# Performance work log

Measured on AMD Instinct MI355X. Metric: run time of the kernel, lower is better.

Reference implementation:

```python
import jax, jax.numpy as jnp
import numpy as np

D = 128  # h_dim == in_dim

def _gat_layer(h, d, src, dst, n_dst, W, U, V, a):
    # h: [N_src, Din], d: [E, 1], src/dst: [E]
    z = h @ W.T          # [N_src, D]
    zi = h @ U.T         # [N_src, D]
    t = d @ V.T          # [E, 1]
    Dh = W.shape[0]
    # attn_fc on concat([z_src, z_dst, t]) split into three partial dots
    e = z[src] @ a[:Dh] + z[dst] @ a[Dh:2 * Dh] + t[:, 0] * a[2 * Dh]
    e = jax.nn.leaky_relu(e)  # [E]
    # segment softmax over incoming edges of each dst node
    m = jax.ops.segment_max(e, dst, num_segments=n_dst)
    ex = jnp.exp(e - m[dst])
    s = jax.ops.segment_sum(ex, dst, num_segments=n_dst)
    alpha = ex / s[dst]  # [E]
    zn = jax.ops.segment_sum(alpha[:, None] * z[src], dst, num_segments=n_dst)
    return jax.nn.relu(zi[:n_dst] + zn)


def setup_inputs() -> dict:
    key = jax.random.key(0)
    ks = jax.random.split(key, 16)
    N0, ND0, ND1 = 100000, 40000, 20000
    E0, E1 = 640000, 320000
    sc = 1.0 / np.sqrt(D)
    inp = {
        "attr": jax.random.normal(ks[0], (N0, D), jnp.float32),
        "d0": jax.random.normal(ks[1], (E0, 1), jnp.float32),
        "d1": jax.random.normal(ks[2], (E1, 1), jnp.float32),
        "src0": jax.random.randint(ks[3], (E0,), 0, N0, jnp.int32),
        "dst0": jax.random.randint(ks[4], (E0,), 0, ND0, jnp.int32),
        "src1": jax.random.randint(ks[5], (E1,), 0, ND0, jnp.int32),
        "dst1": jax.random.randint(ks[6], (E1,), 0, ND1, jnp.int32),
        "n_dst0": ND0,
        "n_dst1": ND1,
        "W0": jax.random.normal(ks[7], (D, D), jnp.float32) * sc,
        "U0": jax.random.normal(ks[8], (D, D), jnp.float32) * sc,
        "V0": jax.random.normal(ks[9], (1, 1), jnp.float32),
        "a0": jax.random.normal(ks[10], (2 * D + 1,), jnp.float32) * sc,
        "W1": jax.random.normal(ks[11], (D, D), jnp.float32) * sc,
        "U1": jax.random.normal(ks[12], (D, D), jnp.float32) * sc,
        "V1": jax.random.normal(ks[13], (1, 1), jnp.float32),
        "a1": jax.random.normal(ks[14], (2 * D + 1,), jnp.float32) * sc,
    }
    return inp


def reference(attr, d0, d1, W0, U0, V0, a0, W1, U1, V1, a1,
              src0, dst0, src1, dst1, n_dst0, n_dst1):
    h = _gat_layer(attr, d0, src0, dst0, n_dst0, W0, U0, V0, a0)
    h = _gat_layer(h, d1, src1, dst1, n_dst1, W1, U1, V1, a1)
    return h
```

## Files before the change

kernel.cpp:

```cpp
#include <hip/hip_runtime.h>
#include <math.h>


#define D 128

typedef __bf16 bf16x8 __attribute__((ext_vector_type(8)));
typedef float f32x4 __attribute__((ext_vector_type(4)));

static __device__ __forceinline__ float lrelu(float x) {
  return x >= 0.f ? x : 0.01f * x;
}
static __device__ __forceinline__ unsigned short f2bf(float v) {
  unsigned int u = __float_as_uint(v);
  u += 0x7fffu + ((u >> 16) & 1u);
  return (unsigned short)(u >> 16);
}
static __device__ __forceinline__ float bf2f(unsigned short b) {
  return __uint_as_float((unsigned int)b << 16);
}

static __device__ __forceinline__ float4 loadV4(const float* p) {
  return *(const float4*)p;
}
static __device__ __forceinline__ float4 loadV4(const unsigned short* p) {
  ushort4 t = *(const ushort4*)p;
  return make_float4(bf2f(t.x), bf2f(t.y), bf2f(t.z), bf2f(t.w));
}
static __device__ __forceinline__ void storeV4(float* p, float4 v) {
  *(float4*)p = v;
}
static __device__ __forceinline__ void storeV4(unsigned short* p, float4 v) {
  ushort4 t;
  t.x = f2bf(v.x);
  t.y = f2bf(v.y);
  t.z = f2bf(v.z);
  t.w = f2bf(v.w);
  *(ushort4*)p = t;
}
static __device__ __forceinline__ void storeZi(float* p, float v) { *p = v; }
static __device__ __forceinline__ void storeZi(unsigned short* p, float v) {
  *p = f2bf(v);
}

static __device__ __forceinline__ int swz(int row, int colb) {
  return row * 256 + (colb ^ ((row & 7) << 4));
}

__global__ __launch_bounds__(256) void cvt4_kernel(
    const float* __restrict__ s0, const float* __restrict__ s1,
    const float* __restrict__ s2, const float* __restrict__ s3,
    __bf16* __restrict__ dst) {
  int idx = blockIdx.x * 256 + threadIdx.x;
  const float* s = (idx < 16384) ? s0
                   : (idx < 32768) ? s1
                   : (idx < 49152) ? s2 : s3;
  dst[idx] = (__bf16)s[idx & 16383];
}

__global__ void zero_int_kernel(int* __restrict__ p, int n) {
  int i = blockIdx.x * 256 + threadIdx.x;
  if (i < n) p[i] = 0;
}

static __device__ __forceinline__ void stageA(const float* A, int rblk,
                                              int rlim, int t,
                                              unsigned char* ldsA) {
  const char* base = (const char*)A + (size_t)rblk * 512;
#pragma unroll
  for (int g = 0; g < 8; ++g) {
    int sb = g * 4096 + t * 16;
    float4 v = make_float4(0.f, 0.f, 0.f, 0.f);
    if (rblk + (sb >> 9) < rlim) v = *(const float4*)(base + sb);
    int db = sb >> 1;
    int row = db >> 8, colb = db & 255;
    ushort4 o;
    o.x = f2bf(v.x);
    o.y = f2bf(v.y);
    o.z = f2bf(v.z);
    o.w = f2bf(v.w);
    *(ushort4*)(&ldsA[swz(row, colb)]) = o;
  }
}
static __device__ __forceinline__ void stageA(const unsigned short* A,
                                              int rblk, int rlim, int t,
                                              unsigned char* ldsA) {
  const char* base = (const char*)A + (size_t)rblk * 256;
#pragma unroll
  for (int g = 0; g < 4; ++g) {
    int bi = g * 4096 + t * 16;
    int row = bi >> 8, colb = bi & 255;
    ushort4 lo = {0, 0, 0, 0}, hi = {0, 0, 0, 0};
    if (rblk + row < rlim) {
      lo = *(const ushort4*)(base + bi);
      hi = *(const ushort4*)(base + bi + 8);
    }
    *(ushort4*)(&ldsA[swz(row, colb)]) = lo;
    *(ushort4*)(&ldsA[swz(row, colb) + 8]) = hi;
  }
}

template <typename AT, typename ZiT>
__global__ __launch_bounds__(256, 3) void gemm_count(
    const AT* __restrict__ A, const __bf16* __restrict__ Wb,
    const __bf16* __restrict__ Ub, unsigned short* __restrict__ z,
    ZiT* __restrict__ zi, const float* __restrict__ a,
    float* __restrict__ zs, float* __restrict__ zd, int n_wb, int rows,
    int ndst, const int* __restrict__ dst0, const int* __restrict__ dst1,
    int* __restrict__ cnt0, int* __restrict__ cnt1, int* __restrict__ rank0,
    int* __restrict__ rank1, int q0, int q1, int IL, int nC) {
  __shared__ unsigned char lds[49152];
  const int blk = blockIdx.x;
  const int t = threadIdx.x;

  if ((blk % IL) == 0 && (blk / IL) < nC) {
    int gid = (blk / IL) * 256 + t;
    const int* dst;
    int* cnt;
    int* rank;
    int i0;
    if (gid < q0) {
      dst = dst0; cnt = cnt0; rank = rank0; i0 = gid * 4;
    } else if (gid < q0 + q1) {
      dst = dst1; cnt = cnt1; rank = rank1; i0 = (gid - q0) * 4;
    } else {
      return;
    }
    int4 d4 = *(const int4*)(dst + i0);
    int4 r4;
    r4.x = atomicAdd(&cnt[d4.x], 1);
    r4.y = atomicAdd(&cnt[d4.y], 1);
    r4.z = atomicAdd(&cnt[d4.z], 1);
    r4.w = atomicAdd(&cnt[d4.w], 1);
    *(int4*)(rank + i0) = r4;
    return;
  }
  const int cb = min(nC, (blk + IL - 1) / IL);
  const int gb = blk - cb;

  const bool isU = (gb >= n_wb);
  const int rblk = (isU ? gb - n_wb : gb) * 64;
  const int rlim = isU ? ndst : rows;
  const __bf16* B = isU ? Ub : Wb;

#pragma unroll
  for (int g = 0; g < 8; ++g) {
    int bi = g * 4096 + t * 16;
    int row = bi >> 8, colb = bi & 255;
    bf16x8 v = *(const bf16x8*)((const char*)B + bi);
    *(bf16x8*)(&lds[swz(row, colb)]) = v;
  }
  stageA(A, rblk, rlim, t, lds + 32768);
  __syncthreads();

  const int wave = t >> 6;
  const int lane = t & 63;
  const int lm = lane & 15;
  const int lk = lane >> 4;
  const int r0 = rblk + wave * 16;
  if (r0 >= rlim) return;

  bf16x8 af[4];
#pragma unroll
  for (int kt = 0; kt < 4; ++kt) {
    int row = wave * 16 + lm;
    af[kt] = *(const bf16x8*)(&lds[32768 + swz(row, kt * 64 + lk * 16)]);
  }

  f32x4 acc[8];
#pragma unroll
  for (int tt = 0; tt < 8; ++tt) acc[tt] = (f32x4){0.f, 0.f, 0.f, 0.f};
#pragma unroll
  for (int kt = 0; kt < 4; ++kt) {
#pragma unroll
    for (int tt = 0; tt < 8; ++tt) {
      int row = tt * 16 + lm;
      bf16x8 bf = *(const bf16x8*)(&lds[swz(row, kt * 64 + lk * 16)]);
      acc[tt] =
          __builtin_amdgcn_mfma_f32_16x16x32_bf16(af[kt], bf, acc[tt], 0, 0, 0);
    }
  }

  if (!isU) {
#pragma unroll
    for (int tt = 0; tt < 8; ++tt)
#pragma unroll
      for (int rr = 0; rr < 4; ++rr)
        z[(size_t)(r0 + lk * 4 + rr) * D + tt * 16 + lm] = f2bf(acc[tt][rr]);

    float p1[4] = {0.f, 0.f, 0.f, 0.f};
    float p2[4] = {0.f, 0.f, 0.f, 0.f};
#pragma unroll
    for (int tt = 0; tt < 8; ++tt) {
      float a1 = a[tt * 16 + lm];
      float a2 = a[D + tt * 16 + lm];
#pragma unroll
      for (int rr = 0; rr < 4; ++rr) {
        p1[rr] += acc[tt][rr] * a1;
        p2[rr] += acc[tt][rr] * a2;
      }
    }
#pragma unroll
    for (int rr = 0; rr < 4; ++rr) {
#pragma unroll
      for (int o = 1; o < 16; o <<= 1) {
        p1[rr] += __shfl_xor(p1[rr], o);
        p2[rr] += __shfl_xor(p2[rr], o);
      }
      if (lm == 0) {
        zs[r0 + lk * 4 + rr] = p1[rr];
        zd[r0 + lk * 4 + rr] = p2[rr];
      }
    }
  } else {
#pragma unroll
    for (int tt = 0; tt < 8; ++tt)
#pragma unroll
      for (int rr = 0; rr < 4; ++rr)
        storeZi(&zi[(size_t)(r0 + lk * 4 + rr) * D + tt * 16 + lm],
                acc[tt][rr]);
  }
}

__global__ __launch_bounds__(256) void scan_partial2(
    const int* __restrict__ cnt0, const int* __restrict__ cnt1,
    int* __restrict__ part, int nb0, int n0, int n1) {
  __shared__ int sm[4];
  int blk = blockIdx.x;
  const int* cnt;
  int* pt;
  int n, lb;
  if (blk < nb0) {
    cnt = cnt0; pt = part; n = n0; lb = blk;
  } else {
    cnt = cnt1; pt = part + 64; n = n1; lb = blk - nb0;
  }
  int base = lb * 1024;
  int t = threadIdx.x;
  int s = 0;
#pragma unroll
  for (int i = 0; i < 4; ++i) {
    int idx = base + t + i * 256;
    s += (idx < n) ? cnt[idx] : 0;
  }
  for (int o = 32; o; o >>= 1) s += __shfl_xor(s, o);
  if ((t & 63) == 0) sm[t >> 6] = s;
  __syncthreads();
  if (t == 0) pt[lb] = sm[0] + sm[1] + sm[2] + sm[3];
}

__global__ __launch_bounds__(256) void scan_final2(
    const int* __restrict__ cnt0, const int* __restrict__ cnt1,
    const int* __restrict__ part, int* __restrict__ offs0,
    int* __restrict__ offs1, int nb0, int n0, int n1, int tot0, int tot1) {
  __shared__ int sm[4];
  __shared__ int sbase;
  int blk = blockIdx.x;
  const int* cnt;
  const int* pt;
  int* offs;
  int n, lb, total;
  if (blk < nb0) {
    cnt = cnt0; pt = part; offs = offs0; n = n0; lb = blk; total = tot0;
  } else {
    cnt = cnt1; pt = part + 64; offs = offs1; n = n1; lb = blk - nb0;
    total = tot1;
  }
  int base = lb * 1024;
  int t = threadIdx.x;
  if (t < 64) {
    int v = (t < lb) ? pt[t] : 0;
#pragma unroll
    for (int o = 32; o; o >>= 1) v += __shfl_xor(v, o);
    if (t == 0) sbase = v;
  }
  int idx = base + t * 4;
  int c0 = (idx + 0 < n) ? cnt[idx + 0] : 0;
  int c1 = (idx + 1 < n) ? cnt[idx + 1] : 0;
  int c2 = (idx + 2 < n) ? cnt[idx + 2] : 0;
  int c3 = (idx + 3 < n) ? cnt[idx + 3] : 0;
  int ts = c0 + c1 + c2 + c3;
  int v = ts;
#pragma unroll
  for (int o = 1; o < 64; o <<= 1) {
    int u = __shfl_up(v, o);
    if ((t & 63) >= o) v += u;
  }
  if ((t & 63) == 63) sm[t >> 6] = v;
  __syncthreads();
  int w = t >> 6;
  int waveoff = 0;
  if (w > 0) waveoff += sm[0];
  if (w > 1) waveoff += sm[1];
  if (w > 2) waveoff += sm[2];
  int run = v - ts + waveoff + sbase;
  if (idx + 0 < n) { offs[idx + 0] = run; run += c0; }
  if (idx + 1 < n) { offs[idx + 1] = run; run += c1; }
  if (idx + 2 < n) { offs[idx + 2] = run; run += c2; }
  if (idx + 3 < n) { offs[idx + 3] = run; run += c3; }
  if (lb == 0 && t == 0) offs[n] = total;
}

__global__ void scatter_w_kernel(const int* __restrict__ src,
                                 const int* __restrict__ dst,
                                 const float* __restrict__ dE,
                                 const float* __restrict__ zs,
                                 const float* __restrict__ zd,
                                 const float* __restrict__ V,
                                 const float* __restrict__ a,
                                 const int* __restrict__ rank,
                                 const int* __restrict__ offs,
                                 int2* __restrict__ csr, int E) {
  int i0 = (blockIdx.x * 256 + threadIdx.x) * 4;
  float vc = V[0] * a[2 * D];
  if (i0 + 4 <= E) {
    int4 s4 = *(const int4*)(src + i0);
    int4 d4 = *(const int4*)(dst + i0);
    float4 de = *(const float4*)(dE + i0);
    int4 r4 = *(const int4*)(rank + i0);
    float zs0 = zs[s4.x], zs1 = zs[s4.y], zs2 = zs[s4.z], zs3 = zs[s4.w];
    float zd0 = zd[d4.x], zd1 = zd[d4.y], zd2 = zd[d4.z], zd3 = zd[d4.w];
    int p0 = offs[d4.x] + r4.x;
    int p1 = offs[d4.y] + r4.y;
    int p2 = offs[d4.z] + r4.z;
    int p3 = offs[d4.w] + r4.w;
    float w0 = __expf(lrelu(zs0 + zd0 + de.x * vc));
    float w1 = __expf(lrelu(zs1 + zd1 + de.y * vc));
    float w2 = __expf(lrelu(zs2 + zd2 + de.z * vc));
    float w3 = __expf(lrelu(zs3 + zd3 + de.w * vc));
    csr[p0] = make_int2(s4.x, __float_as_int(w0));
    csr[p1] = make_int2(s4.y, __float_as_int(w1));
    csr[p2] = make_int2(s4.z, __float_as_int(w2));
    csr[p3] = make_int2(s4.w, __float_as_int(w3));
  } else {
    for (int i = i0; i < E; ++i) {
      int di = dst[i];
      int pp = offs[di] + rank[i];
      float w = __expf(lrelu(zs[src[i]] + zd[di] + dE[i] * vc));
      csr[pp] = make_int2(src[i], __float_as_int(w));
    }
  }
}

template <typename OT>
__global__ __launch_bounds__(256) void gat_perdst(
    const unsigned short* __restrict__ z, const int2* __restrict__ csr,
    const int* __restrict__ offs, const OT* __restrict__ ziin,
    OT* __restrict__ hout, int nd) {
  int n = blockIdx.x * 8 + (threadIdx.x >> 5);
  if (n >= nd) return;
  int lane = threadIdx.x & 31;
  int beg = offs[n], end = offs[n + 1];

  float s0 = 0.f, s1 = 0.f;
  float4 acc0 = make_float4(0.f, 0.f, 0.f, 0.f);
  float4 acc1 = make_float4(0.f, 0.f, 0.f, 0.f);
  const unsigned short* zp = z + lane * 4;
  int j = beg;
  for (; j + 8 <= end; j += 8) {
    int2 pr[8];
#pragma unroll
    for (int u = 0; u < 8; ++u) pr[u] = csr[j + u];
    float4 zv[8];
#pragma unroll
    for (int u = 0; u < 8; ++u) zv[u] = loadV4(zp + (size_t)pr[u].x * D);
#pragma unroll
    for (int u = 0; u < 8; u += 2) {
      float wa = __int_as_float(pr[u].y);
      float wb = __int_as_float(pr[u + 1].y);
      s0 += wa;
      acc0.x += wa * zv[u].x;
      acc0.y += wa * zv[u].y;
      acc0.z += wa * zv[u].z;
      acc0.w += wa * zv[u].w;
      s1 += wb;
      acc1.x += wb * zv[u + 1].x;
      acc1.y += wb * zv[u + 1].y;
      acc1.z += wb * zv[u + 1].z;
      acc1.w += wb * zv[u + 1].w;
    }
  }
  for (; j < end; ++j) {
    int2 pr = csr[j];
    float w = __int_as_float(pr.y);
    float4 zv = loadV4(zp + (size_t)pr.x * D);
    s0 += w;
    acc0.x += w * zv.x;
    acc0.y += w * zv.y;
    acc0.z += w * zv.z;
    acc0.w += w * zv.w;
  }
  float s = s0 + s1;
  float inv = (s > 0.f) ? 1.f / s : 0.f;
  float4 acc = make_float4(acc0.x + acc1.x, acc0.y + acc1.y, acc0.z + acc1.z,
                           acc0.w + acc1.w);
  float4 ziv = loadV4(ziin + (size_t)n * D + lane * 4);
  float4 o4;
  o4.x = fmaxf(ziv.x + acc.x * inv, 0.f);
  o4.y = fmaxf(ziv.y + acc.y * inv, 0.f);
  o4.z = fmaxf(ziv.z + acc.z * inv, 0.f);
  o4.w = fmaxf(ziv.w + acc.w * inv, 0.f);
  storeV4(hout + (size_t)n * D + lane * 4, o4);
}

extern "C" void kernel_launch(void* const* d_in, const int* in_sizes, int n_in,
                              void* d_out, int out_size, void* d_ws,
                              size_t ws_size, hipStream_t stream) {
  const float* attr = (const float*)d_in[0];
  const float* d0 = (const float*)d_in[1];
  const float* d1 = (const float*)d_in[2];
  const int* src0 = (const int*)d_in[3];
  const int* dst0 = (const int*)d_in[4];
  const int* src1 = (const int*)d_in[5];
  const int* dst1 = (const int*)d_in[6];
  const float* W0 = (const float*)d_in[9];
  const float* U0 = (const float*)d_in[10];
  const float* V0 = (const float*)d_in[11];
  const float* a0 = (const float*)d_in[12];
  const float* W1 = (const float*)d_in[13];
  const float* U1 = (const float*)d_in[14];
  const float* V1 = (const float*)d_in[15];
  const float* a1 = (const float*)d_in[16];

  const int N0 = in_sizes[0] / D;
  const int E0 = in_sizes[1];
  const int E1 = in_sizes[2];
  const int ND0 = 40000;
  const int ND1 = 20000;

  char* p = (char*)d_ws;
  auto alloc = [&](size_t bytes) {
    char* q = p;
    p += (bytes + 255) & ~(size_t)255;
    return q;
  };
  unsigned short* z = (unsigned short*)alloc((size_t)N0 * D * 2);
  int2* csr = (int2*)alloc((size_t)E0 * 8);
  unsigned short* h1b = (unsigned short*)alloc((size_t)ND0 * D * 2);
  int* rank0 = (int*)alloc((size_t)E0 * 4);
  int* rank1 = (int*)alloc((size_t)E1 * 4);
  float* zs = (float*)alloc((size_t)N0 * 4);
  float* zd = (float*)alloc((size_t)N0 * 4);
  int* offs0 = (int*)alloc((size_t)(ND0 + 1) * 4);
  int* offs1 = (int*)alloc((size_t)(ND1 + 1) * 4);
  int* cnt01 = (int*)alloc((size_t)(ND0 + ND1) * 4);
  int* part = (int*)alloc((size_t)128 * 4);
  __bf16* wb = (__bf16*)alloc((size_t)4 * D * D * 2);
  int* cnt0 = cnt01;
  int* cnt1 = cnt01 + ND0;
  (void)n_in;
  (void)out_size;
  (void)ws_size;

  float* out = (float*)d_out;

  cvt4_kernel<<<256, 256, 0, stream>>>(W0, U0, W1, U1, wb);
  zero_int_kernel<<<(ND0 + ND1 + 255) / 256, 256, 0, stream>>>(cnt01,
                                                               ND0 + ND1);
  const __bf16* W0b = wb;
  const __bf16* U0b = wb + 16384;
  const __bf16* W1b = wb + 32768;
  const __bf16* U1b = wb + 49152;

  {
    int q0 = E0 / 4, q1 = E1 / 4;
    int nC = (q0 + q1 + 255) / 256;
    int n_wb = (N0 + 63) / 64;
    int n_ub = (ND0 + 63) / 64;
    int nG = n_wb + n_ub;
    int total = nG + nC;
    int IL = total / nC;
    gemm_count<float, unsigned short><<<total, 256, 0, stream>>>(
        attr, W0b, U0b, z, (unsigned short*)d_out, a0, zs, zd, n_wb, N0, ND0,
        dst0, dst1, cnt0, cnt1, rank0, rank1, q0, q1, IL, nC);
  }
  {
    int nb0 = (ND0 + 1023) / 1024;
    int nb1 = (ND1 + 1023) / 1024;
    scan_partial2<<<nb0 + nb1, 256, 0, stream>>>(cnt0, cnt1, part, nb0, ND0,
                                                 ND1);
    scan_final2<<<nb0 + nb1, 256, 0, stream>>>(cnt0, cnt1, part, offs0, offs1,
                                               nb0, ND0, ND1, E0, E1);
  }
  scatter_w_kernel<<<(E0 / 4 + 255) / 256, 256, 0, stream>>>(
      src0, dst0, d0, zs, zd, V0, a0, rank0, offs0, csr, E0);
  gat_perdst<unsigned short><<<(ND0 + 7) / 8, 256, 0, stream>>>(
      z, csr, offs0, (const unsigned short*)d_out, h1b, ND0);

  {
    int n_wb = (ND0 + 63) / 64, n_ub = (ND1 + 63) / 64;
    gemm_count<unsigned short, float><<<n_wb + n_ub, 256, 0, stream>>>(
        h1b, W1b, U1b, z, out, a1, zs, zd, n_wb, ND0, ND1, nullptr, nullptr,
        nullptr, nullptr, nullptr, nullptr, 0, 0, 1, 0);
  }
  scatter_w_kernel<<<(E1 / 4 + 255) / 256, 256, 0, stream>>>(
      src1, dst1, d1, zs, zd, V1, a1, rank1, offs1, csr, E1);
  gat_perdst<float><<<(ND1 + 7) / 8, 256, 0, stream>>>(z, csr, offs1, out, out,
                                                       ND1);
}
```

Before: 154.3 us.

## Move layer-1 edge counting from GEMM kernel into layer-0 scatter kernel

The layer-1 destination counting (atomic rank assignment) now runs inside the layer-0 scatter kernel, interleaved with the scatter blocks, instead of inside the first GEMM kernel. This makes the first GEMM launch lighter and hides the layer-1 counting behind the scatter work. The combined two-graph scans are split into separate per-layer scans, and the layer-1 scan now runs just before layer-1 scatter. This adds two extra kernel launches.

```diff
diff --git a/kernel.cpp b/kernel.cpp
--- a/kernel.cpp
+++ b/kernel.cpp
@@ -44,6 +44,21 @@
 
 static __device__ __forceinline__ int swz(int row, int colb) {
   return row * 256 + (colb ^ ((row & 7) << 4));
+}
+
+static __device__ __forceinline__ void count4(const int* __restrict__ dstC,
+                                              int* __restrict__ cntC,
+                                              int* __restrict__ rankC,
+                                              int gid, int qC) {
+  if (gid >= qC) return;
+  int i0 = gid * 4;
+  int4 d4 = *(const int4*)(dstC + i0);
+  int4 r4;
+  r4.x = atomicAdd(&cntC[d4.x], 1);
+  r4.y = atomicAdd(&cntC[d4.y], 1);
+  r4.z = atomicAdd(&cntC[d4.z], 1);
+  r4.w = atomicAdd(&cntC[d4.w], 1);
+  *(int4*)(rankC + i0) = r4;
 }
 
 __global__ __launch_bounds__(256) void cvt4_kernel(
@@ -105,33 +120,14 @@
     const __bf16* __restrict__ Ub, unsigned short* __restrict__ z,
     ZiT* __restrict__ zi, const float* __restrict__ a,
     float* __restrict__ zs, float* __restrict__ zd, int n_wb, int rows,
-    int ndst, const int* __restrict__ dst0, const int* __restrict__ dst1,
-    int* __restrict__ cnt0, int* __restrict__ cnt1, int* __restrict__ rank0,
-    int* __restrict__ rank1, int q0, int q1, int IL, int nC) {
+    int ndst, const int* __restrict__ dstC, int* __restrict__ cntC,
+    int* __restrict__ rankC, int qC, int IL, int nC) {
   __shared__ unsigned char lds[49152];
   const int blk = blockIdx.x;
   const int t = threadIdx.x;
 
   if ((blk % IL) == 0 && (blk / IL) < nC) {
-    int gid = (blk / IL) * 256 + t;
-    const int* dst;
-    int* cnt;
-    int* rank;
-    int i0;
-    if (gid < q0) {
-      dst = dst0; cnt = cnt0; rank = rank0; i0 = gid * 4;
-    } else if (gid < q0 + q1) {
-      dst = dst1; cnt = cnt1; rank = rank1; i0 = (gid - q0) * 4;
-    } else {
-      return;
-    }
-    int4 d4 = *(const int4*)(dst + i0);
-    int4 r4;
-    r4.x = atomicAdd(&cnt[d4.x], 1);
-    r4.y = atomicAdd(&cnt[d4.y], 1);
-    r4.z = atomicAdd(&cnt[d4.z], 1);
-    r4.w = atomicAdd(&cnt[d4.w], 1);
-    *(int4*)(rank + i0) = r4;
+    count4(dstC, cntC, rankC, (blk / IL) * 256 + t, qC);
     return;
   }
   const int cb = min(nC, (blk + IL - 1) / IL);
@@ -221,20 +217,11 @@
   }
 }
 
-__global__ __launch_bounds__(256) void scan_partial2(
-    const int* __restrict__ cnt0, const int* __restrict__ cnt1,
-    int* __restrict__ part, int nb0, int n0, int n1) {
+__global__ __launch_bounds__(256) void scan_partial(const int* __restrict__ cnt,
+                                                    int* __restrict__ part,
+                                                    int n) {
   __shared__ int sm[4];
-  int blk = blockIdx.x;
-  const int* cnt;
-  int* pt;
-  int n, lb;
-  if (blk < nb0) {
-    cnt = cnt0; pt = part; n = n0; lb = blk;
-  } else {
-    cnt = cnt1; pt = part + 64; n = n1; lb = blk - nb0;
-  }
-  int base = lb * 1024;
+  int base = blockIdx.x * 1024;
   int t = threadIdx.x;
   int s = 0;
 #pragma unroll
@@ -245,30 +232,18 @@
   for (int o = 32; o; o >>= 1) s += __shfl_xor(s, o);
   if ((t & 63) == 0) sm[t >> 6] = s;
   __syncthreads();
-  if (t == 0) pt[lb] = sm[0] + sm[1] + sm[2] + sm[3];
-}
-
-__global__ __launch_bounds__(256) void scan_final2(
-    const int* __restrict__ cnt0, const int* __restrict__ cnt1,
-    const int* __restrict__ part, int* __restrict__ offs0,
-    int* __restrict__ offs1, int nb0, int n0, int n1, int tot0, int tot1) {
+  if (t == 0) part[blockIdx.x] = sm[0] + sm[1] + sm[2] + sm[3];
+}
+
+__global__ __launch_bounds__(256) void scan_final(
+    const int* __restrict__ cnt, const int* __restrict__ part,
+    int* __restrict__ offs, int nb, int n, int total) {
   __shared__ int sm[4];
   __shared__ int sbase;
-  int blk = blockIdx.x;
-  const int* cnt;
-  const int* pt;
-  int* offs;
-  int n, lb, total;
-  if (blk < nb0) {
-    cnt = cnt0; pt = part; offs = offs0; n = n0; lb = blk; total = tot0;
-  } else {
-    cnt = cnt1; pt = part + 64; offs = offs1; n = n1; lb = blk - nb0;
-    total = tot1;
-  }
-  int base = lb * 1024;
+  int base = blockIdx.x * 1024;
   int t = threadIdx.x;
   if (t < 64) {
-    int v = (t < lb) ? pt[t] : 0;
+    int v = (t < nb && t < (int)blockIdx.x) ? part[t] : 0;
 #pragma unroll
     for (int o = 32; o; o >>= 1) v += __shfl_xor(v, o);
     if (t == 0) sbase = v;
@@ -297,20 +272,32 @@
   if (idx + 1 < n) { offs[idx + 1] = run; run += c1; }
   if (idx + 2 < n) { offs[idx + 2] = run; run += c2; }
   if (idx + 3 < n) { offs[idx + 3] = run; run += c3; }
-  if (lb == 0 && t == 0) offs[n] = total;
-}
-
-__global__ void scatter_w_kernel(const int* __restrict__ src,
-                                 const int* __restrict__ dst,
-                                 const float* __restrict__ dE,
-                                 const float* __restrict__ zs,
-                                 const float* __restrict__ zd,
-                                 const float* __restrict__ V,
-                                 const float* __restrict__ a,
-                                 const int* __restrict__ rank,
-                                 const int* __restrict__ offs,
-                                 int2* __restrict__ csr, int E) {
-  int i0 = (blockIdx.x * 256 + threadIdx.x) * 4;
+  if (blockIdx.x == 0 && t == 0) offs[n] = total;
+}
+
+__global__ void scatter_count(const int* __restrict__ src,
+                              const int* __restrict__ dst,
+                              const float* __restrict__ dE,
+                              const float* __restrict__ zs,
+                              const float* __restrict__ zd,
+                              const float* __restrict__ V,
+                              const float* __restrict__ a,
+                              const int* __restrict__ rank,
+                              const int* __restrict__ offs,
+                              int2* __restrict__ csr, int E,
+                              const int* __restrict__ dstC,
+                              int* __restrict__ cntC, int* __restrict__ rankC,
+                              int qC, int IL, int nC) {
+  const int blk = blockIdx.x;
+  const int t = threadIdx.x;
+  if ((blk % IL) == 0 && (blk / IL) < nC) {
+    count4(dstC, cntC, rankC, (blk / IL) * 256 + t, qC);
+    return;
+  }
+  const int cb = min(nC, (blk + IL - 1) / IL);
+  const int sb = blk - cb;
+
+  int i0 = (sb * 256 + t) * 4;
   float vc = V[0] * a[2 * D];
   if (i0 + 4 <= E) {
     int4 s4 = *(const int4*)(src + i0);
@@ -443,7 +430,7 @@
   int* offs0 = (int*)alloc((size_t)(ND0 + 1) * 4);
   int* offs1 = (int*)alloc((size_t)(ND1 + 1) * 4);
   int* cnt01 = (int*)alloc((size_t)(ND0 + ND1) * 4);
-  int* part = (int*)alloc((size_t)128 * 4);
+  int* part = (int*)alloc((size_t)64 * 4);
   __bf16* wb = (__bf16*)alloc((size_t)4 * D * D * 2);
   int* cnt0 = cnt01;
   int* cnt1 = cnt01 + ND0;
@@ -462,27 +449,31 @@
   const __bf16* U1b = wb + 49152;
 
   {
-    int q0 = E0 / 4, q1 = E1 / 4;
-    int nC = (q0 + q1 + 255) / 256;
+    int q0 = E0 / 4;
+    int nC = (q0 + 255) / 256;
     int n_wb = (N0 + 63) / 64;
     int n_ub = (ND0 + 63) / 64;
-    int nG = n_wb + n_ub;
-    int total = nG + nC;
+    int total = n_wb + n_ub + nC;
     int IL = total / nC;
     gemm_count<float, unsigned short><<<total, 256, 0, stream>>>(
         attr, W0b, U0b, z, (unsigned short*)d_out, a0, zs, zd, n_wb, N0, ND0,
-        dst0, dst1, cnt0, cnt1, rank0, rank1, q0, q1, IL, nC);
+        dst0, cnt0, rank0, q0, IL, nC);
   }
   {
-    int nb0 = (ND0 + 1023) / 1024;
-    int nb1 = (ND1 + 1023) / 1024;
-    scan_partial2<<<nb0 + nb1, 256, 0, stream>>>(cnt0, cnt1, part, nb0, ND0,
-                                                 ND1);
-    scan_final2<<<nb0 + nb1, 256, 0, stream>>>(cnt0, cnt1, part, offs0, offs1,
-                                               nb0, ND0, ND1, E0, E1);
-  }
-  scatter_w_kernel<<<(E0 / 4 + 255) / 256, 256, 0, stream>>>(
-      src0, dst0, d0, zs, zd, V0, a0, rank0, offs0, csr, E0);
+    int nb = (ND0 + 1023) / 1024;
+    scan_partial<<<nb, 256, 0, stream>>>(cnt0, part, ND0);
+    scan_final<<<nb, 256, 0, stream>>>(cnt0, part, offs0, nb, ND0, E0);
+  }
+  {
+    int q1 = E1 / 4;
+    int nC = (q1 + 255) / 256;
+    int nS = (E0 / 4 + 255) / 256;
+    int total = nS + nC;
+    int IL = total / nC;
+    scatter_count<<<total, 256, 0, stream>>>(src0, dst0, d0, zs, zd, V0, a0,
+                                             rank0, offs0, csr, E0, dst1,
+                                             cnt1, rank1, q1, IL, nC);
+  }
   gat_perdst<unsigned short><<<(ND0 + 7) / 8, 256, 0, stream>>>(
       z, csr, offs0, (const unsigned short*)d_out, h1b, ND0);
 
@@ -490,10 +481,16 @@
     int n_wb = (ND0 + 63) / 64, n_ub = (ND1 + 63) / 64;
     gemm_count<unsigned short, float><<<n_wb + n_ub, 256, 0, stream>>>(
         h1b, W1b, U1b, z, out, a1, zs, zd, n_wb, ND0, ND1, nullptr, nullptr,
-        nullptr, nullptr, nullptr, nullptr, 0, 0, 1, 0);
-  }
-  scatter_w_kernel<<<(E1 / 4 + 255) / 256, 256, 0, stream>>>(
-      src1, dst1, d1, zs, zd, V1, a1, rank1, offs1, csr, E1);
+        nullptr, 0, 1, 0);
+  }
+  {
+    int nb = (ND1 + 1023) / 1024;
+    scan_partial<<<nb, 256, 0, stream>>>(cnt1, part, ND1);
+    scan_final<<<nb, 256, 0, stream>>>(cnt1, part, offs1, nb, ND1, E1);
+  }
+  scatter_count<<<(E1 / 4 + 255) / 256, 256, 0, stream>>>(
+      src1, dst1, d1, zs, zd, V1, a1, rank1, offs1, csr, E1, nullptr, nullptr,
+      nullptr, 0, 1, 0);
   gat_perdst<float><<<(ND1 + 7) / 8, 256, 0, stream>>>(z, csr, offs1, out, out,
                                                        ND1);
 }
```

After: 156.4 us. Within noise of the previous version (+1.4%).
